# Kernel tuning notes

Measured on AMD Instinct MI355X. Metric: run time of the kernel, lower is better.

The kernel has to match this reference:

```python
import jax, jax.numpy as jnp
import numpy as np

HIDDEN = 1024
D_MEM = 256
BATCH = 4
SEQ = 1024
EPS = 1e-6


def elu_plus_one(x):
    # F.elu(x) + 1 == exp(x) for x<0, x+1 for x>=0 (positive feature map)
    return jnp.where(x > 0, x + 1.0, jnp.exp(x))


def setup_inputs() -> dict:
    key = jax.random.key(0)
    ks = jax.random.split(key, 8)
    hidden_states = jax.random.normal(ks[0], (BATCH, SEQ, HIDDEN), dtype=jnp.float32)
    s = 1.0 / np.sqrt(HIDDEN)
    w_q = jax.random.normal(ks[1], (D_MEM, HIDDEN), dtype=jnp.float32) * s
    w_k = jax.random.normal(ks[2], (D_MEM, HIDDEN), dtype=jnp.float32) * s
    w_v = jax.random.normal(ks[3], (D_MEM, HIDDEN), dtype=jnp.float32) * s
    w_o = jax.random.normal(ks[4], (HIDDEN, D_MEM), dtype=jnp.float32) * (1.0 / np.sqrt(D_MEM))
    gate = jnp.zeros((1,), dtype=jnp.float32)
    # nonzero persistent memory state so retrieval path is exercised
    memory = jax.random.normal(ks[5], (D_MEM, D_MEM), dtype=jnp.float32) * 0.1
    memory_norm = jax.random.uniform(ks[6], (D_MEM,), dtype=jnp.float32) * 10.0 + 1.0
    return {
        "hidden_states": hidden_states,
        "w_q": w_q, "w_k": w_k, "w_v": w_v, "w_o": w_o,
        "gate": gate, "memory": memory, "memory_norm": memory_norm,
    }


def _retrieve(sigma_x, memory, memory_norm):
    # [b,s,d] @ [d,d] -> [b,s,d], normalized by sigma_x @ memory_norm
    a_unnorm = jnp.matmul(sigma_x, memory)
    norm = jnp.clip(jnp.matmul(sigma_x, memory_norm), EPS, None)[..., None]
    out = a_unnorm / norm
    # torch: if memory_norm.sum() < 1e-6 -> zeros
    return jnp.where(memory_norm.sum() < EPS, jnp.zeros_like(out), out)


def reference(hidden_states, w_q, w_k, w_v, w_o, gate, memory, memory_norm):
    b, s, _ = hidden_states.shape
    q = jnp.einsum('bsh,dh->bsd', hidden_states, w_q)
    k = jnp.einsum('bsh,dh->bsd', hidden_states, w_k)
    v = jnp.einsum('bsh,dh->bsd', hidden_states, w_v)

    sigma_q = elu_plus_one(q)
    sigma_k = elu_plus_one(k)

    # --- retrieval from compressive memory ---
    memory_output = _retrieve(sigma_q, memory, memory_norm)

    # --- causal linear attention within segment (cumsum form, as in source) ---
    kv = jnp.einsum('bsd,bse->bsde', sigma_k, v)          # [b,s,d,d]
    kv_cumsum = jnp.cumsum(kv, axis=1)                     # [b,s,d,d]
    k_cumsum = jnp.cumsum(sigma_k, axis=1)                 # [b,s,d]
    numerator = jnp.einsum('bsd,bsde->bse', sigma_q, kv_cumsum)
    denominator = jnp.clip(jnp.einsum('bsd,bsd->bs', sigma_q, k_cumsum), EPS, None)[..., None]
    local_output = numerator / denominator

    g = jax.nn.sigmoid(gate[0])
    combined = g * memory_output + (1.0 - g) * local_output
    output = jnp.einsum('bsd,hd->bsh', combined, w_o)

    # --- delta-rule memory update (detached in torch) ---
    retrieved_unnorm = jnp.matmul(sigma_k, memory)
    norm = jnp.clip(jnp.matmul(sigma_k, memory_norm), EPS, None)[..., None]
    delta_v = v - retrieved_unnorm / norm
    memory_update = jnp.einsum('bsd,bse->de', sigma_k, delta_v) / (b * s)
    new_memory = jax.lax.stop_gradient(memory + memory_update)
    z_update = sigma_k.sum(axis=(0, 1)) / b
    new_memory_norm = jax.lax.stop_gradient(memory_norm + z_update)

    return output, new_memory, new_memory_norm
```

## Files before the change

### kernel.cpp

```cpp
#include <hip/hip_runtime.h>


#define HIDDEN 1024
#define DMEM 256
#define BATCH 4
#define SEQ 1024
#define MTOT (BATCH * SEQ)
#define CHUNK 128
#define NCH (SEQ / CHUNK)
#define NCHT (BATCH * NCH)
#define EPSF 1e-6f

typedef __bf16 bf16x8 __attribute__((ext_vector_type(8)));
typedef __bf16 bf16x4 __attribute__((ext_vector_type(4)));
typedef float f32x4 __attribute__((ext_vector_type(4)));

#define GL_LDS(g, l)                                                                   \
  __builtin_amdgcn_global_load_lds((const __attribute__((address_space(1))) void*)(g), \
                                   (__attribute__((address_space(3))) void*)(l), 16, 0, 0)

__device__ __forceinline__ float elu1(float x) { return x > 0.f ? x + 1.f : __expf(x); }

__device__ __forceinline__ void stage128(const __bf16* p, long ld, int k0, __bf16* sm,
                                         int wave) {
  GL_LDS(p + k0, sm + wave * 512);
  GL_LDS(p + (size_t)64 * ld + k0, sm + 2048 + wave * 512);
  GL_LDS(p + k0 + 32, sm + 4096 + wave * 512);
  GL_LDS(p + (size_t)64 * ld + k0 + 32, sm + 4096 + 2048 + wave * 512);
}
__device__ __forceinline__ void stage64(const __bf16* p, int k0, __bf16* sm, int wave) {
  GL_LDS(p + k0, sm + wave * 512);
  GL_LDS(p + k0 + 32, sm + 2048 + wave * 512);
}

__device__ __forceinline__ void gemm128_bk64(const __bf16* aptr, long lda, const __bf16* bptr,
                                             long ldb, int klen, __bf16* smA, __bf16* smB,
                                             int wave, int wr, int wc, int quad, int l16,
                                             f32x4 (&acc)[4][4]) {
  for (int k0 = 0; k0 < klen; k0 += 64) {
    stage128(aptr, lda, k0, smA, wave);
    stage128(bptr, ldb, k0, smB, wave);
    __syncthreads();
#pragma unroll
    for (int h = 0; h < 2; ++h) {
      bf16x8 aF[4], bF[4];
#pragma unroll
      for (int i = 0; i < 4; ++i)
        aF[i] = *reinterpret_cast<const bf16x8*>(smA + h * 4096 +
                                                 (wr * 64 + i * 16 + l16) * 32 + quad * 8);
#pragma unroll
      for (int j = 0; j < 4; ++j)
        bF[j] = *reinterpret_cast<const bf16x8*>(smB + h * 4096 +
                                                 (wc * 64 + j * 16 + l16) * 32 + quad * 8);
#pragma unroll
      for (int i = 0; i < 4; ++i)
#pragma unroll
        for (int j = 0; j < 4; ++j)
          acc[i][j] = __builtin_amdgcn_mfma_f32_16x16x32_bf16(aF[i], bF[j], acc[i][j], 0, 0, 0);
    }
    __syncthreads();
  }
}

__device__ __forceinline__ void gemm64_bk64(const __bf16* aptr, const __bf16* bptr, long ldb,
                                            int klen, __bf16* smA, __bf16* smB, int wave,
                                            int wr, int wc, int quad, int l16,
                                            f32x4 (&acc)[2][4]) {
  for (int k0 = 0; k0 < klen; k0 += 64) {
    stage64(aptr, k0, smA, wave);
    stage128(bptr, ldb, k0, smB, wave);
    __syncthreads();
#pragma unroll
    for (int h = 0; h < 2; ++h) {
      bf16x8 aF[2], bF[4];
#pragma unroll
      for (int i = 0; i < 2; ++i)
        aF[i] = *reinterpret_cast<const bf16x8*>(smA + h * 2048 +
                                                 (wr * 32 + i * 16 + l16) * 32 + quad * 8);
#pragma unroll
      for (int j = 0; j < 4; ++j)
        bF[j] = *reinterpret_cast<const bf16x8*>(smB + h * 4096 +
                                                 (wc * 64 + j * 16 + l16) * 32 + quad * 8);
#pragma unroll
      for (int i = 0; i < 2; ++i)
#pragma unroll
        for (int j = 0; j < 4; ++j)
          acc[i][j] = __builtin_amdgcn_mfma_f32_16x16x32_bf16(aF[i], bF[j], acc[i][j], 0, 0, 0);
    }
    __syncthreads();
  }
}

__global__ void kprep(const float* __restrict__ hs, const float* __restrict__ wq,
                      const float* __restrict__ wk, const float* __restrict__ wv,
                      const float* __restrict__ wo, const float* __restrict__ mem,
                      __bf16* __restrict__ hsb, __bf16* __restrict__ wqkvb,
                      __bf16* __restrict__ wob, __bf16* __restrict__ memT,
                      float* __restrict__ out) {
  __shared__ float s[64][65];
  int b = blockIdx.x, tid = threadIdx.x;
  if (b < 4096) {
    int i = b * 256 + tid;
    float4 f = reinterpret_cast<const float4*>(hs)[i];
    bf16x4 h = {(__bf16)f.x, (__bf16)f.y, (__bf16)f.z, (__bf16)f.w};
    reinterpret_cast<bf16x4*>(hsb)[i] = h;
  } else if (b < 5120) {
    int y = (b - 4096) >> 8;
    const float* src = (y == 0) ? wq : (y == 1) ? wk : (y == 2) ? wv : wo;
    __bf16* dst = (y < 3) ? wqkvb + (size_t)y * (DMEM * HIDDEN) : wob;
    int i = ((b - 4096) & 255) * 256 + tid;
    float4 f = reinterpret_cast<const float4*>(src)[i];
    bf16x4 h = {(__bf16)f.x, (__bf16)f.y, (__bf16)f.z, (__bf16)f.w};
    reinterpret_cast<bf16x4*>(dst)[i] = h;
  } else if (b < 5136) {
    int t = b - 5120;
    int bx = t & 3, by = t >> 2;
    int r0 = tid >> 6, col = tid & 63;
#pragma unroll
    for (int it = 0; it < 16; ++it) {
      int row = it * 4 + r0;
      s[row][col] = mem[(size_t)(by * 64 + row) * DMEM + bx * 64 + col];
    }
    __syncthreads();
#pragma unroll
    for (int it = 0; it < 16; ++it) {
      int row = it * 4 + r0;
      memT[(size_t)(bx * 64 + row) * DMEM + by * 64 + col] = (__bf16)s[col][row];
    }
  } else {
    int g = (b - 5136) * 256 + tid;
    reinterpret_cast<float4*>(out + (size_t)MTOT * HIDDEN)[g] =
        reinterpret_cast<const float4*>(mem)[g];
  }
}

__global__ __launch_bounds__(256) void k1_qkv_mfma(
    const __bf16* __restrict__ X, const __bf16* __restrict__ W, __bf16* __restrict__ sqb,
    __bf16* __restrict__ skb, __bf16* __restrict__ skT, __bf16* __restrict__ vT) {
  __shared__ __bf16 As[8192];
  __shared__ __bf16 Bs[8192];
  int tid = threadIdx.x;
  int lane = tid & 63, wave = tid >> 6;
  int m0 = blockIdx.x * 128;
  int by = blockIdx.y;
  int wsel = by >> 1, n0 = (by & 1) * 128;
  const __bf16* aptr = X + (size_t)(m0 + (tid >> 2)) * HIDDEN + ((tid & 3) << 3);
  const __bf16* bptr = W + (size_t)(by * 128 + (tid >> 2)) * HIDDEN + ((tid & 3) << 3);
  int wr = wave >> 1, wc = wave & 1, quad = lane >> 4, l16 = lane & 15;
  f32x4 acc[4][4] = {};
  gemm128_bk64(aptr, HIDDEN, bptr, HIDDEN, HIDDEN, As, Bs, wave, wr, wc, quad, l16, acc);
#pragma unroll
  for (int i = 0; i < 4; ++i)
#pragma unroll
    for (int j = 0; j < 4; ++j) {
      int mb = m0 + wr * 64 + i * 16 + quad * 4;
      int n = n0 + wc * 64 + j * 16 + l16;
      if (wsel == 0) {
#pragma unroll
        for (int r = 0; r < 4; ++r) sqb[(size_t)(mb + r) * DMEM + n] = (__bf16)elu1(acc[i][j][r]);
      } else if (wsel == 1) {
        bf16x4 t;
#pragma unroll
        for (int r = 0; r < 4; ++r) {
          float v = elu1(acc[i][j][r]);
          skb[(size_t)(mb + r) * DMEM + n] = (__bf16)v;
          t[r] = (__bf16)v;
        }
        *reinterpret_cast<bf16x4*>(skT + (size_t)n * MTOT + mb) = t;
      } else {
        bf16x4 t;
#pragma unroll
        for (int r = 0; r < 4; ++r) t[r] = (__bf16)acc[i][j][r];
        *reinterpret_cast<bf16x4*>(vT + (size_t)n * MTOT + mb) = t;
      }
    }
}

__global__ __launch_bounds__(256) void kC(const __bf16* __restrict__ vT,
                                          const __bf16* __restrict__ skT,
                                          const __bf16* __restrict__ sqb,
                                          const __bf16* __restrict__ skb,
                                          __bf16* __restrict__ kvcT, __bf16* __restrict__ scb,
                                          float* __restrict__ ksc) {
  __shared__ __bf16 As[8192];
  __shared__ __bf16 Bs[8192];
  int tid = threadIdx.x;
  int c = blockIdx.x;
  int y = blockIdx.y;
  if (y == 6) {
    int d = tid;
    float s = 0.f;
    for (int i = 0; i < CHUNK; ++i) s += (float)skb[(size_t)(c * CHUNK + i) * DMEM + d];
    ksc[c * DMEM + d] = s;
    return;
  }
  int lane = tid & 63, wave = tid >> 6;
  int wr = wave >> 1, wc = wave & 1, quad = lane >> 4, l16 = lane & 15;
  if (y < 4) {
    int e0 = (y >> 1) * 128, d0 = (y & 1) * 128;
    const __bf16* aptr = vT + (size_t)(e0 + (tid >> 2)) * MTOT + c * CHUNK + ((tid & 3) << 3);
    const __bf16* bptr = skT + (size_t)(d0 + (tid >> 2)) * MTOT + c * CHUNK + ((tid & 3) << 3);
    f32x4 acc[4][4] = {};
    gemm128_bk64(aptr, MTOT, bptr, MTOT, CHUNK, As, Bs, wave, wr, wc, quad, l16, acc);
#pragma unroll
    for (int i = 0; i < 4; ++i)
#pragma unroll
      for (int j = 0; j < 4; ++j)
#pragma unroll
        for (int r = 0; r < 4; ++r) {
          int e = e0 + wr * 64 + i * 16 + quad * 4 + r;
          int d = d0 + wc * 64 + j * 16 + l16;
          kvcT[(size_t)c * DMEM * DMEM + (size_t)e * DMEM + d] = (__bf16)acc[i][j][r];
        }
  } else {
    int i0 = (y - 4) * 64;
    const __bf16* aptr = sqb + (size_t)(c * CHUNK + i0 + (tid >> 2)) * DMEM + ((tid & 3) << 3);
    const __bf16* bptr = skb + (size_t)(c * CHUNK + (tid >> 2)) * DMEM + ((tid & 3) << 3);
    f32x4 acc[2][4] = {};
    gemm64_bk64(aptr, bptr, DMEM, DMEM, As, Bs, wave, wr, wc, quad, l16, acc);
#pragma unroll
    for (int i = 0; i < 2; ++i)
#pragma unroll
      for (int j = 0; j < 4; ++j)
#pragma unroll
        for (int r = 0; r < 4; ++r) {
          int ii = i0 + wr * 32 + i * 16 + quad * 4 + r;
          int jj = wc * 64 + j * 16 + l16;
          scb[(size_t)c * CHUNK * CHUNK + (size_t)ii * CHUNK + jj] =
              (jj <= ii) ? (__bf16)acc[i][j][r] : (__bf16)0.f;
        }
  }
}

__global__ __launch_bounds__(256) void kD(const __bf16* __restrict__ kvcT,
                                          __bf16* __restrict__ kvpT,
                                          const float* __restrict__ ksc,
                                          const __bf16* __restrict__ scb,
                                          const __bf16* __restrict__ sqb,
                                          const __bf16* __restrict__ skb,
                                          const float* __restrict__ mnorm,
                                          float* __restrict__ den, float* __restrict__ qn,
                                          float* __restrict__ kn) {
  int vt = blockIdx.x;
  int tid = threadIdx.x;
  if (vt < 128) {
    int batch = vt >> 5;
    size_t idx8 = (size_t)(((vt & 31) * 256 + tid)) * 8;
    float run[8] = {};
    for (int c = 0; c < NCH; ++c) {
      size_t off = (size_t)(batch * NCH + c) * DMEM * DMEM + idx8;
      bf16x8 t = *reinterpret_cast<const bf16x8*>(kvcT + off);
      bf16x8 o;
#pragma unroll
      for (int r = 0; r < 8; ++r) o[r] = (__bf16)run[r];
      *reinterpret_cast<bf16x8*>(kvpT + off) = o;
#pragma unroll
      for (int r = 0; r < 8; ++r) run[r] += (float)t[r];
    }
  } else {
    int wave = tid >> 6, lane = tid & 63;
    int m = (vt - 128) * 4 + wave;
    int c = m >> 7;
    int i = m & 127;
    int cb = c & ~7;
    float s_sc = 0.f, s_d2 = 0.f, s_qn = 0.f, s_kn = 0.f;
    for (int j = lane; j < CHUNK; j += 64)
      s_sc += (float)scb[(size_t)c * CHUNK * CHUNK + (size_t)i * CHUNK + j];
    for (int d = lane; d < DMEM; d += 64) {
      float q = (float)sqb[(size_t)m * DMEM + d];
      float k = (float)skb[(size_t)m * DMEM + d];
      float kp = 0.f;
      for (int cc = cb; cc < c; ++cc) kp += ksc[cc * DMEM + d];
      s_d2 += q * kp;
      s_qn += q * mnorm[d];
      s_kn += k * mnorm[d];
    }
#pragma unroll
    for (int off = 32; off > 0; off >>= 1) {
      s_sc += __shfl_down(s_sc, off);
      s_d2 += __shfl_down(s_d2, off);
      s_qn += __shfl_down(s_qn, off);
      s_kn += __shfl_down(s_kn, off);
    }
    if (lane == 0) {
      den[m] = s_sc + s_d2;
      qn[m] = s_qn;
      kn[m] = s_kn;
    }
  }
}

__global__ __launch_bounds__(256) void kE(const __bf16* __restrict__ scb,
                                          const __bf16* __restrict__ sqb,
                                          const __bf16* __restrict__ skb,
                                          const __bf16* __restrict__ vT,
                                          const __bf16* __restrict__ kvpT,
                                          const __bf16* __restrict__ memT,
                                          const float* __restrict__ den,
                                          const float* __restrict__ qn,
                                          const float* __restrict__ kn,
                                          const float* __restrict__ gate,
                                          const float* __restrict__ mnorm,
                                          __bf16* __restrict__ combb, __bf16* __restrict__ dvT) {
  __shared__ __bf16 As[8192];
  __shared__ __bf16 B1s[8192];
  __shared__ __bf16 B2s[8192];
  __shared__ float flagsh;
  int tid = threadIdx.x;
  int lane = tid & 63, wave = tid >> 6;
  int wr = wave >> 1, wc = wave & 1, quad = lane >> 4, l16 = lane & 15;
  int bid = blockIdx.x;
  if (bid < 128) {
    if (tid == 0) {
      float s = 0.f;
      for (int d = 0; d < DMEM; ++d) s += mnorm[d];
      flagsh = (s < EPSF) ? 0.f : 1.f;
    }
    __syncthreads();
    float fl = flagsh;
    __syncthreads();
    int c = bid >> 2, yy = bid & 3;
    int i0 = (yy >> 1) * 64, e0 = (yy & 1) * 128;
    f32x4 acc_loc[2][4] = {};
    f32x4 acc_mem[2][4] = {};
    {
      const __bf16* aptr =
          scb + (size_t)c * CHUNK * CHUNK + (size_t)(i0 + (tid >> 2)) * CHUNK + ((tid & 3) << 3);
      const __bf16* bptr = vT + (size_t)(e0 + (tid >> 2)) * MTOT + c * CHUNK + ((tid & 3) << 3);
      gemm64_bk64(aptr, bptr, MTOT, CHUNK, As, B1s, wave, wr, wc, quad, l16, acc_loc);
    }
    {
      const __bf16* aptr = sqb + (size_t)(c * CHUNK + i0 + (tid >> 2)) * DMEM + ((tid & 3) << 3);
      const __bf16* b1ptr =
          kvpT + (size_t)c * DMEM * DMEM + (size_t)(e0 + (tid >> 2)) * DMEM + ((tid & 3) << 3);
      const __bf16* b2ptr = memT + (size_t)(e0 + (tid >> 2)) * DMEM + ((tid & 3) << 3);
      for (int k0 = 0; k0 < DMEM; k0 += 64) {
        stage64(aptr, k0, As, wave);
        stage128(b1ptr, DMEM, k0, B1s, wave);
        stage128(b2ptr, DMEM, k0, B2s, wave);
        __syncthreads();
#pragma unroll
        for (int h = 0; h < 2; ++h) {
          bf16x8 aF[2], b1F[4], b2F[4];
#pragma unroll
          for (int i = 0; i < 2; ++i)
            aF[i] = *reinterpret_cast<const bf16x8*>(As + h * 2048 +
                                                     (wr * 32 + i * 16 + l16) * 32 + quad * 8);
#pragma unroll
          for (int j = 0; j < 4; ++j) {
            b1F[j] = *reinterpret_cast<const bf16x8*>(B1s + h * 4096 +
                                                      (wc * 64 + j * 16 + l16) * 32 + quad * 8);
            b2F[j] = *reinterpret_cast<const bf16x8*>(B2s + h * 4096 +
                                                      (wc * 64 + j * 16 + l16) * 32 + quad * 8);
          }
#pragma unroll
          for (int i = 0; i < 2; ++i)
#pragma unroll
            for (int j = 0; j < 4; ++j) {
              acc_loc[i][j] =
                  __builtin_amdgcn_mfma_f32_16x16x32_bf16(aF[i], b1F[j], acc_loc[i][j], 0, 0, 0);
              acc_mem[i][j] =
                  __builtin_amdgcn_mfma_f32_16x16x32_bf16(aF[i], b2F[j], acc_mem[i][j], 0, 0, 0);
            }
        }
        __syncthreads();
      }
    }
    float g = 1.f / (1.f + __expf(-gate[0]));
#pragma unroll
    for (int i = 0; i < 2; ++i) {
      int mb = c * CHUNK + i0 + wr * 32 + i * 16 + quad * 4;
      float dn[4], qv[4];
#pragma unroll
      for (int r = 0; r < 4; ++r) {
        dn[r] = fmaxf(den[mb + r], EPSF);
        qv[r] = fmaxf(qn[mb + r], EPSF);
      }
#pragma unroll
      for (int j = 0; j < 4; ++j) {
        int e = e0 + wc * 64 + j * 16 + l16;
#pragma unroll
        for (int r = 0; r < 4; ++r) {
          float comb = g * fl * acc_mem[i][j][r] / qv[r] + (1.f - g) * acc_loc[i][j][r] / dn[r];
          combb[(size_t)(mb + r) * DMEM + e] = (__bf16)comb;
        }
      }
    }
  } else {
    int t = bid - 128;
    int m0 = (t >> 1) * 128, n0 = (t & 1) * 128;
    const __bf16* aptr = skb + (size_t)(m0 + (tid >> 2)) * DMEM + ((tid & 3) << 3);
    const __bf16* bptr = memT + (size_t)(n0 + (tid >> 2)) * DMEM + ((tid & 3) << 3);
    f32x4 acc[4][4] = {};
    gemm128_bk64(aptr, DMEM, bptr, DMEM, DMEM, As, B1s, wave, wr, wc, quad, l16, acc);
#pragma unroll
    for (int i = 0; i < 4; ++i) {
      int mb = m0 + wr * 64 + i * 16 + quad * 4;
      float kv[4];
#pragma unroll
      for (int r = 0; r < 4; ++r) kv[r] = fmaxf(kn[mb + r], EPSF);
#pragma unroll
      for (int j = 0; j < 4; ++j) {
        int n = n0 + wc * 64 + j * 16 + l16;
        bf16x4 vv = *reinterpret_cast<const bf16x4*>(vT + (size_t)n * MTOT + mb);
        bf16x4 tt;
#pragma unroll
        for (int r = 0; r < 4; ++r) tt[r] = (__bf16)((float)vv[r] - acc[i][j][r] / kv[r]);
        *reinterpret_cast<bf16x4*>(dvT + (size_t)n * MTOT + mb) = tt;
      }
    }
  }
}

__global__ __launch_bounds__(256) void kF(const __bf16* __restrict__ combb,
                                          const __bf16* __restrict__ wob,
                                          const __bf16* __restrict__ skT,
                                          const __bf16* __restrict__ dvT,
                                          const float* __restrict__ ksc,
                                          const float* __restrict__ mnorm,
                                          float* __restrict__ out) {
  __shared__ __bf16 As[8192];
  __shared__ __bf16 Bs[8192];
  int tid = threadIdx.x;
  int bid = blockIdx.x;
  if (bid == 384) {
    int d = tid;
    float s = 0.f;
    for (int c = 0; c < NCHT; ++c) s += ksc[c * DMEM + d];
    out[(size_t)MTOT * HIDDEN + DMEM * DMEM + d] = mnorm[d] + s * (1.f / (float)BATCH);
    return;
  }
  int lane = tid & 63, wave = tid >> 6;
  int wr = wave >> 1, wc = wave & 1, quad = lane >> 4, l16 = lane & 15;
  if (bid < 256) {
    int m0 = (bid & 31) * 128, by = bid >> 5;
    const __bf16* aptr = combb + (size_t)(m0 + (tid >> 2)) * DMEM + ((tid & 3) << 3);
    const __bf16* bptr = wob + (size_t)(by * 128 + (tid >> 2)) * DMEM + ((tid & 3) << 3);
    f32x4 acc[4][4] = {};
    gemm128_bk64(aptr, DMEM, bptr, DMEM, DMEM, As, Bs, wave, wr, wc, quad, l16, acc);
#pragma unroll
    for (int i = 0; i < 4; ++i)
#pragma unroll
      for (int j = 0; j < 4; ++j)
#pragma unroll
        for (int r = 0; r < 4; ++r) {
          int m = m0 + wr * 64 + i * 16 + quad * 4 + r;
          int n = by * 128 + wc * 64 + j * 16 + l16;
          out[(size_t)m * HIDDEN + n] = acc[i][j][r];
        }
  } else {
    int t = bid - 256;
    int kbase = (t >> 3) * 256;
    int yy = t & 7;
    int d0 = (yy >> 1) * 64, e0 = (yy & 1) * 128;
    const __bf16* aptr = skT + (size_t)(d0 + (tid >> 2)) * MTOT + kbase + ((tid & 3) << 3);
    const __bf16* bptr = dvT + (size_t)(e0 + (tid >> 2)) * MTOT + kbase + ((tid & 3) << 3);
    f32x4 acc[2][4] = {};
    gemm64_bk64(aptr, bptr, MTOT, 256, As, Bs, wave, wr, wc, quad, l16, acc);
    float* base = out + (size_t)MTOT * HIDDEN;
#pragma unroll
    for (int i = 0; i < 2; ++i)
#pragma unroll
      for (int j = 0; j < 4; ++j)
#pragma unroll
        for (int r = 0; r < 4; ++r) {
          int d = d0 + wr * 32 + i * 16 + quad * 4 + r;
          int e = e0 + wc * 64 + j * 16 + l16;
          atomicAdd(&base[(size_t)d * DMEM + e], acc[i][j][r] * (1.f / (float)MTOT));
        }
  }
}

extern "C" void kernel_launch(void* const* d_in, const int* in_sizes, int n_in,
                              void* d_out, int out_size, void* d_ws, size_t ws_size,
                              hipStream_t stream) {
  const float* hs = (const float*)d_in[0];
  const float* wq = (const float*)d_in[1];
  const float* wk = (const float*)d_in[2];
  const float* wv = (const float*)d_in[3];
  const float* wo = (const float*)d_in[4];
  const float* gate = (const float*)d_in[5];
  const float* mem = (const float*)d_in[6];
  const float* mnorm = (const float*)d_in[7];
  float* out = (float*)d_out;
  float* ws = (float*)d_ws;

  float* ksc = ws;
  float* den = ksc + 8192;
  float* qn = den + 4096;
  float* kn = qn + 4096;
  __bf16* kvcT = (__bf16*)(ws + 20480);
  __bf16* hsb = kvcT + (size_t)NCHT * DMEM * DMEM;
  __bf16* wqkvb = hsb + (size_t)MTOT * HIDDEN;
  __bf16* wob = wqkvb + (size_t)3 * DMEM * HIDDEN;
  __bf16* memT = wob + (size_t)HIDDEN * DMEM;
  __bf16* sqb = memT + (size_t)DMEM * DMEM;
  __bf16* skb = sqb + (size_t)MTOT * DMEM;
  __bf16* skT = skb + (size_t)MTOT * DMEM;
  __bf16* vT = skT + (size_t)MTOT * DMEM;
  __bf16* scb = vT + (size_t)MTOT * DMEM;
  __bf16* kvpT = scb + (size_t)NCHT * CHUNK * CHUNK;
  __bf16* combb = kvpT + (size_t)NCHT * DMEM * DMEM;
  __bf16* dvT = combb + (size_t)MTOT * DMEM;

  kprep<<<dim3(5152), 256, 0, stream>>>(hs, wq, wk, wv, wo, mem, hsb, wqkvb, wob, memT, out);
  k1_qkv_mfma<<<dim3(32, 6), 256, 0, stream>>>(hsb, wqkvb, sqb, skb, skT, vT);
  kC<<<dim3(NCHT, 7), 256, 0, stream>>>(vT, skT, sqb, skb, kvcT, scb, ksc);
  kD<<<dim3(1152), 256, 0, stream>>>(kvcT, kvpT, ksc, scb, sqb, skb, mnorm, den, qn, kn);
  kE<<<dim3(192), 256, 0, stream>>>(scb, sqb, skb, vT, kvpT, memT, den, qn, kn, gate, mnorm,
                                    combb, dvT);
  kF<<<dim3(385), 256, 0, stream>>>(combb, wob, skT, dvT, ksc, mnorm, out);
}
```

Measured before the change: 146.3 us.

## Fuse chunk KV prefix scan into kC and row reductions into kE

kC's KV-state blocks now loop over the eight chunks of a batch in order. Each block keeps the running prefix in MFMA accumulators and writes the exclusive prefix directly, which removes the separate per-chunk kvcT buffer and the kD scan kernel. The per-row denominator, q·norm and k·norm reductions move into kE's prologue and are held in shared memory. This saves a launch and a full round trip of the per-chunk KV states through global memory. In exchange, the KV stage now runs on only 32 blocks doing serial GEMMs, and kE does extra reduction work before its GEMM.

```diff
diff --git a/kernel.cpp b/kernel.cpp
--- a/kernel.cpp
+++ b/kernel.cpp
@@ -180,14 +180,14 @@
                                           const __bf16* __restrict__ skT,
                                           const __bf16* __restrict__ sqb,
                                           const __bf16* __restrict__ skb,
-                                          __bf16* __restrict__ kvcT, __bf16* __restrict__ scb,
+                                          __bf16* __restrict__ kvpT, __bf16* __restrict__ scb,
                                           float* __restrict__ ksc) {
   __shared__ __bf16 As[8192];
   __shared__ __bf16 Bs[8192];
   int tid = threadIdx.x;
-  int c = blockIdx.x;
-  int y = blockIdx.y;
-  if (y == 6) {
+  int bid = blockIdx.x;
+  if (bid >= 96) {
+    int c = bid - 96;
     int d = tid;
     float s = 0.f;
     for (int i = 0; i < CHUNK; ++i) s += (float)skb[(size_t)(c * CHUNK + i) * DMEM + d];
@@ -196,24 +196,34 @@
   }
   int lane = tid & 63, wave = tid >> 6;
   int wr = wave >> 1, wc = wave & 1, quad = lane >> 4, l16 = lane & 15;
-  if (y < 4) {
-    int e0 = (y >> 1) * 128, d0 = (y & 1) * 128;
-    const __bf16* aptr = vT + (size_t)(e0 + (tid >> 2)) * MTOT + c * CHUNK + ((tid & 3) << 3);
-    const __bf16* bptr = skT + (size_t)(d0 + (tid >> 2)) * MTOT + c * CHUNK + ((tid & 3) << 3);
-    f32x4 acc[4][4] = {};
-    gemm128_bk64(aptr, MTOT, bptr, MTOT, CHUNK, As, Bs, wave, wr, wc, quad, l16, acc);
-#pragma unroll
-    for (int i = 0; i < 4; ++i)
-#pragma unroll
-      for (int j = 0; j < 4; ++j)
-#pragma unroll
-        for (int r = 0; r < 4; ++r) {
-          int e = e0 + wr * 64 + i * 16 + quad * 4 + r;
-          int d = d0 + wc * 64 + j * 16 + l16;
-          kvcT[(size_t)c * DMEM * DMEM + (size_t)e * DMEM + d] = (__bf16)acc[i][j][r];
-        }
+  if (bid < 32) {
+    int batch = bid >> 3;
+    int e0 = ((bid >> 1) & 3) * 64;
+    int d0 = (bid & 1) * 128;
+    int c0 = batch * NCH;
+    const __bf16* aptr =
+        vT + (size_t)(e0 + (tid >> 2)) * MTOT + batch * SEQ + ((tid & 3) << 3);
+    const __bf16* bptr =
+        skT + (size_t)(d0 + (tid >> 2)) * MTOT + batch * SEQ + ((tid & 3) << 3);
+    f32x4 run[2][4] = {};
+    for (int cc = 0; cc < NCH; ++cc) {
+      __bf16* dst = kvpT + (size_t)(c0 + cc) * DMEM * DMEM;
+#pragma unroll
+      for (int i = 0; i < 2; ++i)
+#pragma unroll
+        for (int j = 0; j < 4; ++j)
+#pragma unroll
+          for (int r = 0; r < 4; ++r) {
+            int e = e0 + wr * 32 + i * 16 + quad * 4 + r;
+            int d = d0 + wc * 64 + j * 16 + l16;
+            dst[(size_t)e * DMEM + d] = (__bf16)run[i][j][r];
+          }
+      gemm64_bk64(aptr + cc * CHUNK, bptr + cc * CHUNK, MTOT, CHUNK, As, Bs, wave, wr, wc,
+                  quad, l16, run);
+    }
   } else {
-    int i0 = (y - 4) * 64;
+    int sb = bid - 32;
+    int c = sb >> 1, i0 = (sb & 1) * 64;
     const __bf16* aptr = sqb + (size_t)(c * CHUNK + i0 + (tid >> 2)) * DMEM + ((tid & 3) << 3);
     const __bf16* bptr = skb + (size_t)(c * CHUNK + (tid >> 2)) * DMEM + ((tid & 3) << 3);
     f32x4 acc[2][4] = {};
@@ -229,64 +239,6 @@
           scb[(size_t)c * CHUNK * CHUNK + (size_t)ii * CHUNK + jj] =
               (jj <= ii) ? (__bf16)acc[i][j][r] : (__bf16)0.f;
         }
-  }
-}
-
-__global__ __launch_bounds__(256) void kD(const __bf16* __restrict__ kvcT,
-                                          __bf16* __restrict__ kvpT,
-                                          const float* __restrict__ ksc,
-                                          const __bf16* __restrict__ scb,
-                                          const __bf16* __restrict__ sqb,
-                                          const __bf16* __restrict__ skb,
-                                          const float* __restrict__ mnorm,
-                                          float* __restrict__ den, float* __restrict__ qn,
-                                          float* __restrict__ kn) {
-  int vt = blockIdx.x;
-  int tid = threadIdx.x;
-  if (vt < 128) {
-    int batch = vt >> 5;
-    size_t idx8 = (size_t)(((vt & 31) * 256 + tid)) * 8;
-    float run[8] = {};
-    for (int c = 0; c < NCH; ++c) {
-      size_t off = (size_t)(batch * NCH + c) * DMEM * DMEM + idx8;
-      bf16x8 t = *reinterpret_cast<const bf16x8*>(kvcT + off);
-      bf16x8 o;
-#pragma unroll
-      for (int r = 0; r < 8; ++r) o[r] = (__bf16)run[r];
-      *reinterpret_cast<bf16x8*>(kvpT + off) = o;
-#pragma unroll
-      for (int r = 0; r < 8; ++r) run[r] += (float)t[r];
-    }
-  } else {
-    int wave = tid >> 6, lane = tid & 63;
-    int m = (vt - 128) * 4 + wave;
-    int c = m >> 7;
-    int i = m & 127;
-    int cb = c & ~7;
-    float s_sc = 0.f, s_d2 = 0.f, s_qn = 0.f, s_kn = 0.f;
-    for (int j = lane; j < CHUNK; j += 64)
-      s_sc += (float)scb[(size_t)c * CHUNK * CHUNK + (size_t)i * CHUNK + j];
-    for (int d = lane; d < DMEM; d += 64) {
-      float q = (float)sqb[(size_t)m * DMEM + d];
-      float k = (float)skb[(size_t)m * DMEM + d];
-      float kp = 0.f;
-      for (int cc = cb; cc < c; ++cc) kp += ksc[cc * DMEM + d];
-      s_d2 += q * kp;
-      s_qn += q * mnorm[d];
-      s_kn += k * mnorm[d];
-    }
-#pragma unroll
-    for (int off = 32; off > 0; off >>= 1) {
-      s_sc += __shfl_down(s_sc, off);
-      s_d2 += __shfl_down(s_d2, off);
-      s_qn += __shfl_down(s_qn, off);
-      s_kn += __shfl_down(s_kn, off);
-    }
-    if (lane == 0) {
-      den[m] = s_sc + s_d2;
-      qn[m] = s_qn;
-      kn[m] = s_kn;
-    }
   }
 }
 
@@ -296,31 +248,53 @@
                                           const __bf16* __restrict__ vT,
                                           const __bf16* __restrict__ kvpT,
                                           const __bf16* __restrict__ memT,
-                                          const float* __restrict__ den,
-                                          const float* __restrict__ qn,
-                                          const float* __restrict__ kn,
+                                          const float* __restrict__ ksc,
                                           const float* __restrict__ gate,
                                           const float* __restrict__ mnorm,
                                           __bf16* __restrict__ combb, __bf16* __restrict__ dvT) {
   __shared__ __bf16 As[8192];
   __shared__ __bf16 B1s[8192];
   __shared__ __bf16 B2s[8192];
+  __shared__ float rowA[128];
+  __shared__ float rowB[64];
   __shared__ float flagsh;
   int tid = threadIdx.x;
   int lane = tid & 63, wave = tid >> 6;
   int wr = wave >> 1, wc = wave & 1, quad = lane >> 4, l16 = lane & 15;
   int bid = blockIdx.x;
   if (bid < 128) {
-    if (tid == 0) {
-      float s = 0.f;
-      for (int d = 0; d < DMEM; ++d) s += mnorm[d];
-      flagsh = (s < EPSF) ? 0.f : 1.f;
-    }
-    __syncthreads();
-    float fl = flagsh;
-    __syncthreads();
     int c = bid >> 2, yy = bid & 3;
     int i0 = (yy >> 1) * 64, e0 = (yy & 1) * 128;
+    {
+      if (tid == 0) {
+        float s = 0.f;
+        for (int d = 0; d < DMEM; ++d) s += mnorm[d];
+        flagsh = (s < EPSF) ? 0.f : 1.f;
+      }
+      int r = tid >> 2, p = tid & 3;
+      int m = c * CHUNK + i0 + r;
+      int cb = c & ~(NCH - 1);
+      float ssc = 0.f;
+      for (int jj = p * 32; jj < p * 32 + 32; ++jj)
+        ssc += (float)scb[(size_t)c * CHUNK * CHUNK + (size_t)(i0 + r) * CHUNK + jj];
+      float sd2 = 0.f, sqn = 0.f;
+      for (int d = p * 64; d < p * 64 + 64; ++d) {
+        float q = (float)sqb[(size_t)m * DMEM + d];
+        float kp = 0.f;
+        for (int ccx = cb; ccx < c; ++ccx) kp += ksc[ccx * DMEM + d];
+        sd2 += q * kp;
+        sqn += q * mnorm[d];
+      }
+      float dsum = ssc + sd2;
+      dsum += __shfl_xor(dsum, 1);
+      dsum += __shfl_xor(dsum, 2);
+      sqn += __shfl_xor(sqn, 1);
+      sqn += __shfl_xor(sqn, 2);
+      if (p == 0) {
+        rowA[r] = fmaxf(dsum, EPSF);
+        rowB[r] = fmaxf(sqn, EPSF);
+      }
+    }
     f32x4 acc_loc[2][4] = {};
     f32x4 acc_mem[2][4] = {};
     {
@@ -367,14 +341,16 @@
       }
     }
     float g = 1.f / (1.f + __expf(-gate[0]));
+    float fl = flagsh;
 #pragma unroll
     for (int i = 0; i < 2; ++i) {
-      int mb = c * CHUNK + i0 + wr * 32 + i * 16 + quad * 4;
+      int lrow = wr * 32 + i * 16 + quad * 4;
+      int mb = c * CHUNK + i0 + lrow;
       float dn[4], qv[4];
 #pragma unroll
       for (int r = 0; r < 4; ++r) {
-        dn[r] = fmaxf(den[mb + r], EPSF);
-        qv[r] = fmaxf(qn[mb + r], EPSF);
+        dn[r] = rowA[lrow + r];
+        qv[r] = rowB[lrow + r];
       }
 #pragma unroll
       for (int j = 0; j < 4; ++j) {
@@ -389,16 +365,26 @@
   } else {
     int t = bid - 128;
     int m0 = (t >> 1) * 128, n0 = (t & 1) * 128;
+    {
+      int r = tid >> 1, p = tid & 1;
+      int m = m0 + r;
+      float skn = 0.f;
+      for (int d = p * 128; d < p * 128 + 128; ++d)
+        skn += (float)skb[(size_t)m * DMEM + d] * mnorm[d];
+      skn += __shfl_xor(skn, 1);
+      if (p == 0) rowA[r] = fmaxf(skn, EPSF);
+    }
     const __bf16* aptr = skb + (size_t)(m0 + (tid >> 2)) * DMEM + ((tid & 3) << 3);
     const __bf16* bptr = memT + (size_t)(n0 + (tid >> 2)) * DMEM + ((tid & 3) << 3);
     f32x4 acc[4][4] = {};
     gemm128_bk64(aptr, DMEM, bptr, DMEM, DMEM, As, B1s, wave, wr, wc, quad, l16, acc);
 #pragma unroll
     for (int i = 0; i < 4; ++i) {
-      int mb = m0 + wr * 64 + i * 16 + quad * 4;
+      int lrow = wr * 64 + i * 16 + quad * 4;
+      int mb = m0 + lrow;
       float kv[4];
 #pragma unroll
-      for (int r = 0; r < 4; ++r) kv[r] = fmaxf(kn[mb + r], EPSF);
+      for (int r = 0; r < 4; ++r) kv[r] = rowA[lrow + r];
 #pragma unroll
       for (int j = 0; j < 4; ++j) {
         int n = n0 + wc * 64 + j * 16 + l16;
@@ -486,11 +472,7 @@
   float* ws = (float*)d_ws;
 
   float* ksc = ws;
-  float* den = ksc + 8192;
-  float* qn = den + 4096;
-  float* kn = qn + 4096;
-  __bf16* kvcT = (__bf16*)(ws + 20480);
-  __bf16* hsb = kvcT + (size_t)NCHT * DMEM * DMEM;
+  __bf16* hsb = (__bf16*)(ws + 8192);
   __bf16* wqkvb = hsb + (size_t)MTOT * HIDDEN;
   __bf16* wob = wqkvb + (size_t)3 * DMEM * HIDDEN;
   __bf16* memT = wob + (size_t)HIDDEN * DMEM;
@@ -505,9 +487,8 @@
 
   kprep<<<dim3(5152), 256, 0, stream>>>(hs, wq, wk, wv, wo, mem, hsb, wqkvb, wob, memT, out);
   k1_qkv_mfma<<<dim3(32, 6), 256, 0, stream>>>(hsb, wqkvb, sqb, skb, skT, vT);
-  kC<<<dim3(NCHT, 7), 256, 0, stream>>>(vT, skT, sqb, skb, kvcT, scb, ksc);
-  kD<<<dim3(1152), 256, 0, stream>>>(kvcT, kvpT, ksc, scb, sqb, skb, mnorm, den, qn, kn);
-  kE<<<dim3(192), 256, 0, stream>>>(scb, sqb, skb, vT, kvpT, memT, den, qn, kn, gate, mnorm,
-                                    combb, dvT);
+  kC<<<dim3(128), 256, 0, stream>>>(vT, skT, sqb, skb, kvpT, scb, ksc);
+  kE<<<dim3(192), 256, 0, stream>>>(scb, sqb, skb, vT, kvpT, memT, ksc, gate, mnorm, combb,
+                                    dvT);
   kF<<<dim3(385), 256, 0, stream>>>(combb, wob, skT, dvT, ksc, mnorm, out);
 }
```

Measured after the change: 198.7 us. 1.36x slower.
